# Optimization experiments

Hardware: AMD Instinct MI355X
Metric: run time of the kernel (lower is better)

The kernel has to match this reference:

```python
import jax, jax.numpy as jnp
import numpy as np

_J6 = jnp.array([[0, 0, 0, 0, 0, 1], [0, 0, 0, 0, -1, 0], [0, 0, 0, 1, 0, 0],
                 [0, 0, 1, 0, 0, 0], [0, -1, 0, 0, 0, 0], [1, 0, 0, 0, 0, 0]], dtype=jnp.float32)
_PAIRS4 = [(0, 1), (0, 2), (0, 3), (1, 2), (1, 3), (2, 3)]


def exterior(p1, p2):
    # p1, p2: (B,T,H,4) -> (B,T,H,6) normalized Pluecker line coordinates
    parts = [p1[..., i] * p2[..., j] - p1[..., j] * p2[..., i] for i, j in _PAIRS4]
    L = jnp.stack(parts, axis=-1)
    n = jnp.sqrt(jnp.sum(L * L, axis=-1, keepdims=True))
    return L / jnp.maximum(n, 1e-12)


def setup_inputs() -> dict:
    D, H = 1024, 16
    B, T = 2, 2048
    key = jax.random.key(0)
    ks = jax.random.split(key, 16)
    s = 0.02
    return {
        'x': jax.random.normal(ks[0], (B, T, D), dtype=jnp.float32),
        'qkv_w': jax.random.normal(ks[1], (D, 3 * D), dtype=jnp.float32) * s,
        'qkv_b': jnp.zeros((3 * D,), dtype=jnp.float32),
        'w1_write': jax.random.normal(ks[2], (D, 4 * H), dtype=jnp.float32) * s,
        'w2_write': jax.random.normal(ks[3], (D, 4 * H), dtype=jnp.float32) * s,
        'w1_read': jax.random.normal(ks[4], (D, 4 * H), dtype=jnp.float32) * s,
        'w2_read': jax.random.normal(ks[5], (D, 4 * H), dtype=jnp.float32) * s,
        'geo_w': jax.random.normal(ks[6], (D, D), dtype=jnp.float32) * s,
        'geo_b': jnp.zeros((D,), dtype=jnp.float32),
        'gate_w': jax.random.normal(ks[7], (D, H), dtype=jnp.float32) * s,
        'gate_b': jnp.zeros((H,), dtype=jnp.float32),
        'inc_scale': jnp.ones((H,), dtype=jnp.float32),
        'out_w': jax.random.normal(ks[8], (D, D), dtype=jnp.float32) * s,
        'out_b': jnp.zeros((D,), dtype=jnp.float32),
    }


def reference(x, qkv_w, qkv_b, w1_write, w2_write, w1_read, w2_read,
              geo_w, geo_b, gate_w, gate_b, inc_scale, out_w, out_b):
    B, T, D = x.shape
    H = inc_scale.shape[0]
    dh = D // H
    scale = dh ** -0.5

    qkv = (x @ qkv_w + qkv_b).reshape(B, T, 3, H, dh)
    qkv = jnp.transpose(qkv, (2, 0, 3, 1, 4))  # (3,B,H,T,dh)
    q, k, v = qkv[0], qkv[1], qkv[2]

    std_logits = jnp.einsum('bhqd,bhkd->bhqk', q, k) * scale

    x_prev = jnp.concatenate([jnp.zeros((B, 1, D), dtype=x.dtype), x[:, :-1]], axis=1)
    w1 = (x_prev @ w1_write).reshape(B, T, H, 4)
    w2 = (x @ w2_write).reshape(B, T, H, 4)
    write_lines = exterior(w1, w2)  # (B,T,H,6)
    r1 = (x @ w1_read).reshape(B, T, H, 4)
    r2 = (x @ w2_read).reshape(B, T, H, 4)
    read_lines = exterior(r1, r2)  # (B,T,H,6)

    J_write = jnp.einsum('bthi,ij->bthj', write_lines, _J6)  # (B,T,H,6)
    geo_logits = jnp.einsum('bqhi,bkhi->bhqk', read_lines, J_write)
    geo_logits = geo_logits * inc_scale.reshape(1, H, 1, 1)

    mask = jnp.triu(jnp.ones((T, T), dtype=bool), k=1)  # True above diagonal
    neg = jnp.float32(-jnp.inf)

    std_attn = jax.nn.softmax(jnp.where(mask, neg, std_logits), axis=-1)
    std_out = jnp.einsum('bhqk,bhkd->bqhd', std_attn, v).reshape(B, T, D)

    geo_attn = jax.nn.softmax(jnp.where(mask, neg, geo_logits), axis=-1)
    geo_v = (x @ geo_w + geo_b).reshape(B, T, H, dh)
    geo_out = jnp.einsum('bhqk,bkhd->bqhd', geo_attn, geo_v).reshape(B, T, D)

    gate = jax.nn.sigmoid(x @ gate_w + gate_b)  # (B,T,H)
    gate = jnp.mean(gate, axis=-1, keepdims=True)  # (B,T,1)

    combined = (1.0 - gate) * std_out + gate * geo_out
    return combined @ out_w + out_b
```

## Files before the change

kernel.cpp:

```cpp
#include <hip/hip_runtime.h>
#include <hip/hip_bf16.h>

#define Bc 2
#define Tc 2048
#define Dc 1024
#define Hc 16
#define Mc (Bc*Tc)
#define QB 64
#define KB 32
#define NALL 4480

typedef __attribute__((ext_vector_type(8))) short bf16x8;
typedef __attribute__((ext_vector_type(4))) short bf16x4;
typedef __attribute__((ext_vector_type(4))) float fx4;

__device__ __forceinline__ short f2bf(float f) {
  __hip_bfloat16 h = __float2bfloat16(f);
  return *reinterpret_cast<short*>(&h);
}
__device__ __forceinline__ float bf2f(short s) {
  unsigned int u = ((unsigned int)(unsigned short)s) << 16;
  float f;
  __builtin_memcpy(&f, &u, 4);
  return f;
}

#define MFMA(a, b, c) __builtin_amdgcn_mfma_f32_16x16x32_bf16((a), (b), (c), 0, 0, 0)

#define GLD16(G, L) __builtin_amdgcn_global_load_lds( \
    (const __attribute__((address_space(1))) unsigned int*)(G), \
    (__attribute__((address_space(3))) unsigned int*)(L), 16, 0, 0)

__global__ __launch_bounds__(256) void f2b_k(const float* __restrict__ in,
                                             short* __restrict__ out) {
  const int i = blockIdx.x * 256 + threadIdx.x;
  const float4 v = ((const float4*)in)[i];
  bf16x4 o;
  o[0] = f2bf(v.x); o[1] = f2bf(v.y); o[2] = f2bf(v.z); o[3] = f2bf(v.w);
  ((bf16x4*)out)[i] = o;
}

__global__ void biasall_k(const float* __restrict__ qkv_b,
                          const float* __restrict__ geob,
                          const float* __restrict__ gateb,
                          float* __restrict__ ball) {
  const int n = blockIdx.x * 256 + threadIdx.x;
  if (n >= NALL) return;
  float v = 0.f;
  if (n < 1024)      v = qkv_b[n] * 0.125f;
  else if (n < 3072) v = qkv_b[n];
  else if (n < 4096) v = geob[n - 3072];
  else if (n >= 4352 && n < 4368) v = gateb[n - 4352];
  ball[n] = v;
}

__global__ __launch_bounds__(256) void tconv_all_k(
    const float* __restrict__ qkv_w, const float* __restrict__ geow,
    const float* __restrict__ w1w, const float* __restrict__ w2w,
    const float* __restrict__ w1r, const float* __restrict__ w2r,
    const float* __restrict__ gatew, short* __restrict__ wtall)
{
  __shared__ float tile[32][33];
  const int n0 = blockIdx.x * 32, k0 = blockIdx.y * 32;
  const int tx = threadIdx.x & 31, ty = threadIdx.x >> 5;
  const int n = n0 + tx;
  const float* src = nullptr; int ln = 0, sN = 0;
  if (n < 3072)      { src = qkv_w; ln = n;        sN = 3072; }
  else if (n < 4096) { src = geow;  ln = n - 3072; sN = 1024; }
  else if (n < 4160) { src = w1w;   ln = n - 4096; sN = 64; }
  else if (n < 4224) { src = w2w;   ln = n - 4160; sN = 64; }
  else if (n < 4288) { src = w1r;   ln = n - 4224; sN = 64; }
  else if (n < 4352) { src = w2r;   ln = n - 4288; sN = 64; }
  else if (n < 4368) { src = gatew; ln = n - 4352; sN = 16; }
  #pragma unroll
  for (int i = 0; i < 4; i++)
    tile[ty * 4 + i][tx] = src ? src[(size_t)(k0 + ty * 4 + i) * sN + ln] : 0.f;
  __syncthreads();
  #pragma unroll
  for (int i = 0; i < 4; i++) {
    const int nn = n0 + ty * 4 + i;
    const float s = (nn < 1024) ? 0.125f : 1.f;
    wtall[(size_t)nn * 1024 + k0 + tx] = f2bf(tile[tx][ty * 4 + i] * s);
  }
}

__global__ __launch_bounds__(256) void tconv_k(const float* __restrict__ W,
                                               short* __restrict__ Wt,
                                               int K, int N) {
  __shared__ float tile[32][33];
  const int k0 = blockIdx.y * 32, n0 = blockIdx.x * 32;
  const int tx = threadIdx.x & 31, ty = threadIdx.x >> 5;
  #pragma unroll
  for (int i = 0; i < 4; i++)
    tile[ty * 4 + i][tx] = W[(size_t)(k0 + ty * 4 + i) * N + n0 + tx];
  __syncthreads();
  #pragma unroll
  for (int i = 0; i < 4; i++)
    Wt[(size_t)(n0 + ty * 4 + i) * K + k0 + tx] = f2bf(tile[tx][ty * 4 + i]);
}

template<bool BF16_OUT>
__global__ __launch_bounds__(256) void gemm_mfma_k(
    const short* __restrict__ A, const short* __restrict__ Bt,
    const float* __restrict__ bias, void* __restrict__ Cv,
    int M, int N, int K)
{
  __shared__ short As[128][32];
  __shared__ short Bs[128][32];
  const int m0 = blockIdx.y * 128, n0 = blockIdx.x * 128;
  const int tid = threadIdx.x;
  const int wave = tid >> 6, lane = tid & 63;
  const int l15 = lane & 15, lg = lane >> 4;
  const int wm = wave >> 1, wn = wave & 1;
  const int srow = lane >> 2;
  const int schk = (lane & 3) * 8;

  const size_t aBase = (size_t)(m0 + wave * 16 + srow) * K + schk;
  const size_t bBase = (size_t)(n0 + wave * 16 + srow) * K + schk;

  fx4 acc[4][4] = {};

  for (int k0 = 0; k0 < K; k0 += 32) {
    __syncthreads();
    GLD16(&A[aBase + k0],              &As[wave * 16][0]);
    GLD16(&A[aBase + (size_t)64 * K + k0], &As[64 + wave * 16][0]);
    GLD16(&Bt[bBase + k0],             &Bs[wave * 16][0]);
    GLD16(&Bt[bBase + (size_t)64 * K + k0], &Bs[64 + wave * 16][0]);
    __syncthreads();
    bf16x8 af[4], bf[4];
    #pragma unroll
    for (int i = 0; i < 4; i++) {
      af[i] = *(const bf16x8*)&As[wm * 64 + i * 16 + l15][8 * lg];
      bf[i] = *(const bf16x8*)&Bs[wn * 64 + i * 16 + l15][8 * lg];
    }
    #pragma unroll
    for (int i = 0; i < 4; i++)
      #pragma unroll
      for (int j = 0; j < 4; j++)
        acc[i][j] = MFMA(af[i], bf[j], acc[i][j]);
  }

  #pragma unroll
  for (int i = 0; i < 4; i++)
    #pragma unroll
    for (int j = 0; j < 4; j++) {
      const int n = n0 + wn * 64 + j * 16 + l15;
      const float bv = bias ? bias[n] : 0.f;
      #pragma unroll
      for (int rg = 0; rg < 4; rg++) {
        const int m = m0 + wm * 64 + i * 16 + lg * 4 + rg;
        const float v = acc[i][j][rg] + bv;
        if constexpr (BF16_OUT)
          ((short*)Cv)[(size_t)m * N + n] = f2bf(v);
        else
          ((float*)Cv)[(size_t)m * N + n] = v;
      }
    }
}

__device__ __forceinline__ void exterior6(const float a[4], const float c[4], float L[6]) {
  L[0] = a[0]*c[1] - a[1]*c[0];
  L[1] = a[0]*c[2] - a[2]*c[0];
  L[2] = a[0]*c[3] - a[3]*c[0];
  L[3] = a[1]*c[2] - a[2]*c[1];
  L[4] = a[1]*c[3] - a[3]*c[1];
  L[5] = a[2]*c[3] - a[3]*c[2];
}

__device__ __forceinline__ void load4bf(const short* p, float o[4]) {
  const bf16x4 v = *(const bf16x4*)p;
  o[0] = bf2f(v[0]); o[1] = bf2f(v[1]); o[2] = bf2f(v[2]); o[3] = bf2f(v[3]);
}

__global__ void lines_k(const short* __restrict__ allb,
                        const float* __restrict__ incs,
                        short* __restrict__ JWb, short* __restrict__ RLb)
{
  const int idx = blockIdx.x * 256 + threadIdx.x;
  if (idx >= Bc * Tc * Hc) return;
  const int h = idx & 15;
  const int t = (idx >> 4) & (Tc - 1);
  const int b = idx >> 15;
  const size_t row = (size_t)b * Tc + t;
  const size_t lrow = ((size_t)(b * Hc + h) * Tc + t) * 8;

  float a[4] = {0.f, 0.f, 0.f, 0.f};
  float c[4];
  load4bf(&allb[row * NALL + 4160 + h * 4], c);
  if (t > 0) load4bf(&allb[(row - 1) * NALL + 4096 + h * 4], a);

  float L[6];
  exterior6(a, c, L);
  float n = sqrtf(L[0]*L[0] + L[1]*L[1] + L[2]*L[2] + L[3]*L[3] + L[4]*L[4] + L[5]*L[5]);
  float inv = 1.f / fmaxf(n, 1e-12f);
  const float s = incs[h];
  bf16x8 jw;
  jw[0] = f2bf( L[5] * inv * s);
  jw[1] = f2bf(-L[4] * inv * s);
  jw[2] = f2bf( L[3] * inv * s);
  jw[3] = f2bf( L[2] * inv * s);
  jw[4] = f2bf(-L[1] * inv * s);
  jw[5] = f2bf( L[0] * inv * s);
  jw[6] = 0; jw[7] = 0;
  *(bf16x8*)&JWb[lrow] = jw;

  load4bf(&allb[row * NALL + 4224 + h * 4], a);
  load4bf(&allb[row * NALL + 4288 + h * 4], c);
  exterior6(a, c, L);
  n = sqrtf(L[0]*L[0] + L[1]*L[1] + L[2]*L[2] + L[3]*L[3] + L[4]*L[4] + L[5]*L[5]);
  inv = 1.f / fmaxf(n, 1e-12f);
  bf16x8 rl;
  #pragma unroll
  for (int i = 0; i < 6; i++) rl[i] = f2bf(L[i] * inv);
  rl[6] = 0; rl[7] = 0;
  *(bf16x8*)&RLb[lrow] = rl;
}

__global__ void gate_k(const short* __restrict__ allb, float* __restrict__ gate) {
  const int idx = blockIdx.x * 256 + threadIdx.x;
  if (idx >= Mc) return;
  float ssum = 0.f;
  #pragma unroll
  for (int hh = 0; hh < 16; hh++) {
    const float v = bf2f(allb[(size_t)idx * NALL + 4352 + hh]);
    ssum += 1.f / (1.f + __expf(-v));
  }
  gate[idx] = ssum * (1.f / 16.f);
}

#define LOADK(K0, a0, a1, b0, b1) { \
  const size_t rb0 = (size_t)(b * Tc + (K0) + l15) * NALL + 1024 + h * 64; \
  const size_t rb1 = rb0 + (size_t)16 * NALL; \
  a0 = *(const bf16x8*)&allb[rb0 + lg * 8]; \
  a1 = *(const bf16x8*)&allb[rb0 + 32 + lg * 8]; \
  b0 = *(const bf16x8*)&allb[rb1 + lg * 8]; \
  b1 = *(const bf16x8*)&allb[rb1 + 32 + lg * 8]; }

#define LOADJW(K0, j0, j1) { \
  j0 = z8; j1 = z8; \
  if (lg == 0) { \
    j0 = *(const bf16x8*)&JWb[(size_t)(bh * Tc + (K0) + l15) * 8]; \
    j1 = *(const bf16x8*)&JWb[(size_t)(bh * Tc + (K0) + 16 + l15) * 8]; \
  } }

#define LOADVG(K0, vr, gr) { \
  vr = *(const bf16x8*)&allb[(size_t)(b * Tc + (K0) + kk) * NALL + 2048 + h * 64 + dg]; \
  gr = *(const bf16x8*)&allb[(size_t)(b * Tc + (K0) + kk) * NALL + 3072 + h * 64 + dg]; }

#define STAGEVG(CUR, vr, gr) { \
  _Pragma("unroll") for (int j = 0; j < 8; j++) { \
    const int d = dg + j; \
    const int col = ((kc2 ^ ((d >> 3) & 3)) << 3) | kl2; \
    Vt[CUR][d][col] = vr[j]; Gt[CUR][d][col] = gr[j]; \
  } }

#define COMPUTE(K0, CUR, ka0, ka1, kb0, kb1, jw0, jw1) \
  if ((K0) <= qhi) { \
    fx4 z = {0.f, 0.f, 0.f, 0.f}; \
    fx4 sS0, sS1, sG0, sG1; \
    __builtin_amdgcn_s_setprio(1); \
    sS0 = MFMA(qf0, ka0, z); sS0 = MFMA(qf1, ka1, sS0); \
    sS1 = MFMA(qf0, kb0, z); sS1 = MFMA(qf1, kb1, sS1); \
    sG0 = MFMA(rlf, jw0, z); sG1 = MFMA(rlf, jw1, z); \
    __builtin_amdgcn_s_setprio(0); \
    if ((K0) + KB - 1 > q0 + wave * 16) { \
      const int kg0 = (K0) + l15, kg1 = (K0) + 16 + l15; \
      _Pragma("unroll") for (int r = 0; r < 4; r++) { \
        const int qg = q0 + wave * 16 + lg * 4 + r; \
        if (kg0 > qg) { sS0[r] = -1e30f; sG0[r] = -1e30f; } \
        if (kg1 > qg) { sS1[r] = -1e30f; sG1[r] = -1e30f; } \
      } } \
    _Pragma("unroll") for (int r = 0; r < 4; r++) { \
      const int ql = lg * 4 + r; \
      const float p0 = __expf(sS0[r]); const float p1 = __expf(sS1[r]); \
      lpS[r] += p0 + p1; \
      Ps[wave][ql][l15] = f2bf(p0); Ps[wave][ql][16 + l15] = f2bf(p1); \
      const float g0 = __expf(sG0[r]); const float g1 = __expf(sG1[r]); \
      lpG[r] += g0 + g1; \
      Pg[wave][ql][l15] = f2bf(g0); Pg[wave][ql][16 + l15] = f2bf(g1); \
    } \
    const bf16x8 pa  = *(const bf16x8*)&Ps[wave][l15][8 * lg]; \
    const bf16x8 pga = *(const bf16x8*)&Pg[wave][l15][8 * lg]; \
    __builtin_amdgcn_s_setprio(1); \
    _Pragma("unroll") for (int dt = 0; dt < 4; dt++) { \
      const int dV = dt * 16 + l15; \
      const int swz = 8 * (lg ^ ((dV >> 3) & 3)); \
      accS[dt] = MFMA(pa,  *(const bf16x8*)&Vt[CUR][dV][swz], accS[dt]); \
      accG[dt] = MFMA(pga, *(const bf16x8*)&Gt[CUR][dV][swz], accG[dt]); \
    } \
    __builtin_amdgcn_s_setprio(0); \
  }

__global__ __launch_bounds__(256) void attn3_k(
    const short* __restrict__ allb,
    const short* __restrict__ RLb,
    const short* __restrict__ JWb,
    const float* __restrict__ gate,
    short* __restrict__ combb)
{
  const int orig = blockIdx.x;
  const int xcd  = orig & 7;
  const int idx  = orig >> 3;
  const int pairIdx = idx & 15;
  const int bh   = xcd + 8 * (idx >> 4);
  const int b = bh >> 4, h = bh & 15;
  const int tid = threadIdx.x;
  const int wave = tid >> 6;
  const int lane = tid & 63;
  const int l15 = lane & 15;
  const int lg  = lane >> 4;
  const int kk  = tid >> 3;
  const int dg  = (tid & 7) * 8;
  const int kc2 = kk >> 3, kl2 = kk & 7;

  __shared__ short Vt[2][64][40];
  __shared__ short Gt[2][64][40];
  __shared__ short Ps[4][16][40];
  __shared__ short Pg[4][16][40];

  const bf16x8 z8 = {0, 0, 0, 0, 0, 0, 0, 0};

  for (int half = 0; half < 2; half++) {
    const int qt = half ? (31 - pairIdx) : pairIdx;
    const int q0 = qt * QB;
    const int nkt = 2 * qt + 2;
    const int qrow = wave * 16 + l15;
    const int qhi = q0 + wave * 16 + 15;

    const size_t qrb = (size_t)(b * Tc + q0 + qrow) * NALL + h * 64;
    const bf16x8 qf0 = *(const bf16x8*)&allb[qrb + lg * 8];
    const bf16x8 qf1 = *(const bf16x8*)&allb[qrb + 32 + lg * 8];
    bf16x8 rlf = z8;
    if (lg == 0) rlf = *(const bf16x8*)&RLb[(size_t)(bh * Tc + q0 + qrow) * 8];

    fx4 accS[4] = {}, accG[4] = {};
    float lpS[4] = {0.f, 0.f, 0.f, 0.f};
    float lpG[4] = {0.f, 0.f, 0.f, 0.f};

    bf16x8 kA0a, kA1a, kB0a, kB1a, jw0a, jw1a, vrA, grA;
    bf16x8 kA0b, kA1b, kB0b, kB1b, jw0b, jw1b, vrB, grB;
    LOADK(0, kA0a, kA1a, kB0a, kB1a);
    LOADJW(0, jw0a, jw1a);
    LOADVG(0, vrA, grA);

    __syncthreads();

    for (int kt = 0; kt < nkt; kt += 2) {
      const int k0a = kt * KB, k0b = k0a + KB;
      STAGEVG(0, vrA, grA);
      LOADK(k0b, kA0b, kA1b, kB0b, kB1b);
      LOADJW(k0b, jw0b, jw1b);
      LOADVG(k0b, vrB, grB);
      __syncthreads();
      COMPUTE(k0a, 0, kA0a, kA1a, kB0a, kB1a, jw0a, jw1a);
      STAGEVG(1, vrB, grB);
      if (kt + 2 < nkt) {
        LOADK(k0b + KB, kA0a, kA1a, kB0a, kB1a);
        LOADJW(k0b + KB, jw0a, jw1a);
        LOADVG(k0b + KB, vrA, grA);
      }
      __syncthreads();
      COMPUTE(k0b, 1, kA0b, kA1b, kB0b, kB1b, jw0b, jw1b);
    }

    #pragma unroll
    for (int r = 0; r < 4; r++) {
      float ls = lpS[r];
      ls += __shfl_xor(ls, 1); ls += __shfl_xor(ls, 2);
      ls += __shfl_xor(ls, 4); ls += __shfl_xor(ls, 8);
      float lgeo = lpG[r];
      lgeo += __shfl_xor(lgeo, 1); lgeo += __shfl_xor(lgeo, 2);
      lgeo += __shfl_xor(lgeo, 4); lgeo += __shfl_xor(lgeo, 8);
      const int qg = q0 + wave * 16 + lg * 4 + r;
      const float gt = gate[(size_t)b * Tc + qg];
      const float invS = (1.f - gt) / ls;
      const float invG = gt / lgeo;
      #pragma unroll
      for (int dt = 0; dt < 4; dt++) {
        const float o = accS[dt][r] * invS + accG[dt][r] * invG;
        combb[(size_t)(b * Tc + qg) * 1024 + h * 64 + dt * 16 + l15] = f2bf(o);
      }
    }
  }
}

extern "C" void kernel_launch(void* const* d_in, const int* in_sizes, int n_in,
                              void* d_out, int out_size, void* d_ws, size_t ws_size,
                              hipStream_t stream) {
  (void)in_sizes; (void)n_in; (void)out_size; (void)ws_size;
  const float* x     = (const float*)d_in[0];
  const float* qkv_w = (const float*)d_in[1];
  const float* qkv_b = (const float*)d_in[2];
  const float* w1w   = (const float*)d_in[3];
  const float* w2w   = (const float*)d_in[4];
  const float* w1r   = (const float*)d_in[5];
  const float* w2r   = (const float*)d_in[6];
  const float* geow  = (const float*)d_in[7];
  const float* geob  = (const float*)d_in[8];
  const float* gatew = (const float*)d_in[9];
  const float* gateb = (const float*)d_in[10];
  const float* incs  = (const float*)d_in[11];
  const float* outw  = (const float*)d_in[12];
  const float* outb  = (const float*)d_in[13];
  float* out = (float*)d_out;

  char* p = (char*)d_ws;
  short* xb    = (short*)p;  p += (size_t)4096 * 1024 * 2;
  short* wtall = (short*)p;  p += (size_t)NALL * 1024 * 2;
  short* allb  = (short*)p;  p += (size_t)4096 * NALL * 2;
  short* combb = (short*)p;  p += (size_t)4096 * 1024 * 2;
  short* wtout = (short*)p;  p += (size_t)1024 * 1024 * 2;
  short* JWb   = (short*)p;  p += (size_t)32 * 2048 * 8 * 2;
  short* RLb   = (short*)p;  p += (size_t)32 * 2048 * 8 * 2;
  float* ball  = (float*)p;  p += (size_t)NALL * 4;
  float* gatev = (float*)p;  p += (size_t)4096 * 4;

  const dim3 blk(256);

  f2b_k<<<dim3(4096), blk, 0, stream>>>(x, xb);
  biasall_k<<<dim3((NALL + 255) / 256), blk, 0, stream>>>(qkv_b, geob, gateb, ball);
  tconv_all_k<<<dim3(NALL / 32, 32), blk, 0, stream>>>(qkv_w, geow, w1w, w2w, w1r, w2r, gatew, wtall);
  tconv_k<<<dim3(32, 32), blk, 0, stream>>>(outw, wtout, 1024, 1024);

  gemm_mfma_k<true><<<dim3(NALL / 128, 32), blk, 0, stream>>>(xb, wtall, ball, allb, 4096, NALL, 1024);

  lines_k<<<dim3((Bc * Tc * Hc + 255) / 256), blk, 0, stream>>>(allb, incs, JWb, RLb);
  gate_k<<<dim3((Mc + 255) / 256), blk, 0, stream>>>(allb, gatev);

  attn3_k<<<dim3(512), blk, 0, stream>>>(allb, RLb, JWb, gatev, combb);

  gemm_mfma_k<false><<<dim3(8, 32), blk, 0, stream>>>(combb, wtout, outb, (void*)out, 4096, 1024, 1024);
}
```

Measured before the change: 210.7 us.

## Pre-transpose V/geo-V to global, give each wave its own 32-query tile

Adds a kernel that transposes the V and geo-V slices into a per-head, d-major layout, so the attention kernel can load PV operands directly from global memory into registers instead of staging them through LDS with block-wide barriers. The attention kernel is restructured so each wave independently handles a 32-row query tile (two 16-row subtiles sharing the K loads) with no __syncthreads, and work is balanced by reversing the tile order. Log2e is folded into the Q scale and incidence scale so exp2f replaces __expf. This costs an extra transpose pass and more global reads per wave in exchange for removing synchronization and shared-memory staging.

```diff
diff --git a/kernel.cpp b/kernel.cpp
--- a/kernel.cpp
+++ b/kernel.cpp
@@ -6,9 +6,10 @@
 #define Dc 1024
 #define Hc 16
 #define Mc (Bc*Tc)
-#define QB 64
 #define KB 32
 #define NALL 4480
+#define QSCALE 0.18033688056680776f
+#define LOG2E  1.4426950408889634f
 
 typedef __attribute__((ext_vector_type(8))) short bf16x8;
 typedef __attribute__((ext_vector_type(4))) short bf16x4;
@@ -47,7 +48,7 @@
   const int n = blockIdx.x * 256 + threadIdx.x;
   if (n >= NALL) return;
   float v = 0.f;
-  if (n < 1024)      v = qkv_b[n] * 0.125f;
+  if (n < 1024)      v = qkv_b[n] * QSCALE;
   else if (n < 3072) v = qkv_b[n];
   else if (n < 4096) v = geob[n - 3072];
   else if (n >= 4352 && n < 4368) v = gateb[n - 4352];
@@ -79,7 +80,7 @@
   #pragma unroll
   for (int i = 0; i < 4; i++) {
     const int nn = n0 + ty * 4 + i;
-    const float s = (nn < 1024) ? 0.125f : 1.f;
+    const float s = (nn < 1024) ? QSCALE : 1.f;
     wtall[(size_t)nn * 1024 + k0 + tx] = f2bf(tile[tx][ty * 4 + i] * s);
   }
 }
@@ -158,6 +159,29 @@
     }
 }
 
+__global__ __launch_bounds__(256) void vgt_k(const short* __restrict__ allb,
+                                             short* __restrict__ vgt) {
+  const int t0 = blockIdx.x * 64;
+  const int bh = blockIdx.y;
+  const int path = blockIdx.z;
+  const int b = bh >> 4, h = bh & 15;
+  __shared__ short tile[64][66];
+  const int tt = threadIdx.x >> 2;
+  const int dc = (threadIdx.x & 3) * 16;
+  const size_t src = (size_t)(b * Tc + t0 + tt) * NALL + (path ? 3072 : 2048) + h * 64 + dc;
+  *(bf16x8*)&tile[tt][dc]     = *(const bf16x8*)&allb[src];
+  *(bf16x8*)&tile[tt][dc + 8] = *(const bf16x8*)&allb[src + 8];
+  __syncthreads();
+  const int dd = threadIdx.x >> 2;
+  const int tc = (threadIdx.x & 3) * 16;
+  bf16x8 o0, o1;
+  #pragma unroll
+  for (int j = 0; j < 8; j++) { o0[j] = tile[tc + j][dd]; o1[j] = tile[tc + 8 + j][dd]; }
+  const size_t dst = ((size_t)(path * 32 + bh) * 64 + dd) * Tc + t0 + tc;
+  *(bf16x8*)&vgt[dst]     = o0;
+  *(bf16x8*)&vgt[dst + 8] = o1;
+}
+
 __device__ __forceinline__ void exterior6(const float a[4], const float c[4], float L[6]) {
   L[0] = a[0]*c[1] - a[1]*c[0];
   L[1] = a[0]*c[2] - a[2]*c[0];
@@ -193,7 +217,7 @@
   exterior6(a, c, L);
   float n = sqrtf(L[0]*L[0] + L[1]*L[1] + L[2]*L[2] + L[3]*L[3] + L[4]*L[4] + L[5]*L[5]);
   float inv = 1.f / fmaxf(n, 1e-12f);
-  const float s = incs[h];
+  const float s = incs[h] * LOG2E;
   bf16x8 jw;
   jw[0] = f2bf( L[5] * inv * s);
   jw[1] = f2bf(-L[4] * inv * s);
@@ -228,160 +252,153 @@
   gate[idx] = ssum * (1.f / 16.f);
 }
 
-#define LOADK(K0, a0, a1, b0, b1) { \
+#define LOADKJ4(K0, k00, k01, k10, k11, j0, j1) { \
   const size_t rb0 = (size_t)(b * Tc + (K0) + l15) * NALL + 1024 + h * 64; \
   const size_t rb1 = rb0 + (size_t)16 * NALL; \
-  a0 = *(const bf16x8*)&allb[rb0 + lg * 8]; \
-  a1 = *(const bf16x8*)&allb[rb0 + 32 + lg * 8]; \
-  b0 = *(const bf16x8*)&allb[rb1 + lg * 8]; \
-  b1 = *(const bf16x8*)&allb[rb1 + 32 + lg * 8]; }
-
-#define LOADJW(K0, j0, j1) { \
+  k00 = *(const bf16x8*)&allb[rb0 + lg * 8]; \
+  k01 = *(const bf16x8*)&allb[rb0 + 32 + lg * 8]; \
+  k10 = *(const bf16x8*)&allb[rb1 + lg * 8]; \
+  k11 = *(const bf16x8*)&allb[rb1 + 32 + lg * 8]; \
   j0 = z8; j1 = z8; \
   if (lg == 0) { \
     j0 = *(const bf16x8*)&JWb[(size_t)(bh * Tc + (K0) + l15) * 8]; \
     j1 = *(const bf16x8*)&JWb[(size_t)(bh * Tc + (K0) + 16 + l15) * 8]; \
   } }
 
-#define LOADVG(K0, vr, gr) { \
-  vr = *(const bf16x8*)&allb[(size_t)(b * Tc + (K0) + kk) * NALL + 2048 + h * 64 + dg]; \
-  gr = *(const bf16x8*)&allb[(size_t)(b * Tc + (K0) + kk) * NALL + 3072 + h * 64 + dg]; }
-
-#define STAGEVG(CUR, vr, gr) { \
-  _Pragma("unroll") for (int j = 0; j < 8; j++) { \
-    const int d = dg + j; \
-    const int col = ((kc2 ^ ((d >> 3) & 3)) << 3) | kl2; \
-    Vt[CUR][d][col] = vr[j]; Gt[CUR][d][col] = gr[j]; \
-  } }
-
-#define COMPUTE(K0, CUR, ka0, ka1, kb0, kb1, jw0, jw1) \
-  if ((K0) <= qhi) { \
-    fx4 z = {0.f, 0.f, 0.f, 0.f}; \
-    fx4 sS0, sS1, sG0, sG1; \
-    __builtin_amdgcn_s_setprio(1); \
-    sS0 = MFMA(qf0, ka0, z); sS0 = MFMA(qf1, ka1, sS0); \
-    sS1 = MFMA(qf0, kb0, z); sS1 = MFMA(qf1, kb1, sS1); \
-    sG0 = MFMA(rlf, jw0, z); sG1 = MFMA(rlf, jw1, z); \
-    __builtin_amdgcn_s_setprio(0); \
-    if ((K0) + KB - 1 > q0 + wave * 16) { \
-      const int kg0 = (K0) + l15, kg1 = (K0) + 16 + l15; \
+#define LOADVG4(K0, vf, gf) { \
+  const size_t vb = ((size_t)bh * 64 + l15) * Tc + (K0) + lg * 8; \
+  const size_t gb = vb + (size_t)32 * 64 * Tc; \
+  vf[0] = *(const bf16x8*)&vgt[vb]; \
+  vf[1] = *(const bf16x8*)&vgt[vb + (size_t)16 * Tc]; \
+  vf[2] = *(const bf16x8*)&vgt[vb + (size_t)32 * Tc]; \
+  vf[3] = *(const bf16x8*)&vgt[vb + (size_t)48 * Tc]; \
+  gf[0] = *(const bf16x8*)&vgt[gb]; \
+  gf[1] = *(const bf16x8*)&vgt[gb + (size_t)16 * Tc]; \
+  gf[2] = *(const bf16x8*)&vgt[gb + (size_t)32 * Tc]; \
+  gf[3] = *(const bf16x8*)&vgt[gb + (size_t)48 * Tc]; }
+
+#define COMPUTE4(K0, k00, k01, k10, k11, j0, j1, vf, gf) { \
+  const fx4 z = {0.f, 0.f, 0.f, 0.f}; \
+  fx4 sS[2][2], sG[2][2]; \
+  __builtin_amdgcn_s_setprio(1); \
+  sS[0][0] = MFMA(qf[0][0], k00, z); sS[0][0] = MFMA(qf[0][1], k01, sS[0][0]); \
+  sS[0][1] = MFMA(qf[0][0], k10, z); sS[0][1] = MFMA(qf[0][1], k11, sS[0][1]); \
+  sS[1][0] = MFMA(qf[1][0], k00, z); sS[1][0] = MFMA(qf[1][1], k01, sS[1][0]); \
+  sS[1][1] = MFMA(qf[1][0], k10, z); sS[1][1] = MFMA(qf[1][1], k11, sS[1][1]); \
+  sG[0][0] = MFMA(rlf[0], j0, z); sG[0][1] = MFMA(rlf[0], j1, z); \
+  sG[1][0] = MFMA(rlf[1], j0, z); sG[1][1] = MFMA(rlf[1], j1, z); \
+  __builtin_amdgcn_s_setprio(0); \
+  if ((K0) == q0) { \
+    _Pragma("unroll") for (int sq = 0; sq < 2; sq++) \
+    _Pragma("unroll") for (int st = 0; st < 2; st++) { \
+      const int kg = (K0) + st * 16 + l15; \
       _Pragma("unroll") for (int r = 0; r < 4; r++) { \
-        const int qg = q0 + wave * 16 + lg * 4 + r; \
-        if (kg0 > qg) { sS0[r] = -1e30f; sG0[r] = -1e30f; } \
-        if (kg1 > qg) { sS1[r] = -1e30f; sG1[r] = -1e30f; } \
-      } } \
+        const int qg = q0 + sq * 16 + lg * 4 + r; \
+        if (kg > qg) { sS[sq][st][r] = -1e30f; sG[sq][st][r] = -1e30f; } \
+      } } } \
+  _Pragma("unroll") for (int sq = 0; sq < 2; sq++) { \
     _Pragma("unroll") for (int r = 0; r < 4; r++) { \
       const int ql = lg * 4 + r; \
-      const float p0 = __expf(sS0[r]); const float p1 = __expf(sS1[r]); \
-      lpS[r] += p0 + p1; \
-      Ps[wave][ql][l15] = f2bf(p0); Ps[wave][ql][16 + l15] = f2bf(p1); \
-      const float g0 = __expf(sG0[r]); const float g1 = __expf(sG1[r]); \
-      lpG[r] += g0 + g1; \
-      Pg[wave][ql][l15] = f2bf(g0); Pg[wave][ql][16 + l15] = f2bf(g1); \
-    } \
-    const bf16x8 pa  = *(const bf16x8*)&Ps[wave][l15][8 * lg]; \
-    const bf16x8 pga = *(const bf16x8*)&Pg[wave][l15][8 * lg]; \
-    __builtin_amdgcn_s_setprio(1); \
+      const float p0 = exp2f(sS[sq][0][r]); \
+      const float p1 = exp2f(sS[sq][1][r]); \
+      lpS[sq][r] += p0 + p1; \
+      Ps[wave][sq][ql][l15]      = f2bf(p0); \
+      Ps[wave][sq][ql][16 + l15] = f2bf(p1); \
+      const float g0 = exp2f(sG[sq][0][r]); \
+      const float g1 = exp2f(sG[sq][1][r]); \
+      lpG[sq][r] += g0 + g1; \
+      Pg[wave][sq][ql][l15]      = f2bf(g0); \
+      Pg[wave][sq][ql][16 + l15] = f2bf(g1); \
+    } } \
+  __builtin_amdgcn_s_setprio(1); \
+  _Pragma("unroll") for (int sq = 0; sq < 2; sq++) { \
+    const bf16x8 pa  = *(const bf16x8*)&Ps[wave][sq][l15][8 * lg]; \
+    const bf16x8 pga = *(const bf16x8*)&Pg[wave][sq][l15][8 * lg]; \
     _Pragma("unroll") for (int dt = 0; dt < 4; dt++) { \
-      const int dV = dt * 16 + l15; \
-      const int swz = 8 * (lg ^ ((dV >> 3) & 3)); \
-      accS[dt] = MFMA(pa,  *(const bf16x8*)&Vt[CUR][dV][swz], accS[dt]); \
-      accG[dt] = MFMA(pga, *(const bf16x8*)&Gt[CUR][dV][swz], accG[dt]); \
-    } \
-    __builtin_amdgcn_s_setprio(0); \
-  }
-
-__global__ __launch_bounds__(256) void attn3_k(
+      accS[sq][dt] = MFMA(pa,  vf[dt], accS[sq][dt]); \
+      accG[sq][dt] = MFMA(pga, gf[dt], accG[sq][dt]); \
+    } } \
+  __builtin_amdgcn_s_setprio(0); }
+
+__global__ __launch_bounds__(256) void attn4_k(
     const short* __restrict__ allb,
+    const short* __restrict__ vgt,
     const short* __restrict__ RLb,
     const short* __restrict__ JWb,
     const float* __restrict__ gate,
     short* __restrict__ combb)
 {
   const int orig = blockIdx.x;
-  const int xcd  = orig & 7;
-  const int idx  = orig >> 3;
-  const int pairIdx = idx & 15;
-  const int bh   = xcd + 8 * (idx >> 4);
+  const int xcd = orig & 7;
+  const int g = orig >> 3;
+  const int bh = xcd + 8 * (g >> 4);
+  const int blkIn = g & 15;
+  const int tid = threadIdx.x;
+  const int wave = tid >> 6, lane = tid & 63;
+  const int l15 = lane & 15, lg = lane >> 4;
+  const int qs = 63 - (blkIn * 4 + wave);
   const int b = bh >> 4, h = bh & 15;
-  const int tid = threadIdx.x;
-  const int wave = tid >> 6;
-  const int lane = tid & 63;
-  const int l15 = lane & 15;
-  const int lg  = lane >> 4;
-  const int kk  = tid >> 3;
-  const int dg  = (tid & 7) * 8;
-  const int kc2 = kk >> 3, kl2 = kk & 7;
-
-  __shared__ short Vt[2][64][40];
-  __shared__ short Gt[2][64][40];
-  __shared__ short Ps[4][16][40];
-  __shared__ short Pg[4][16][40];
+  const int q0 = qs * 32;
+
+  __shared__ short Ps[4][2][16][40];
+  __shared__ short Pg[4][2][16][40];
 
   const bf16x8 z8 = {0, 0, 0, 0, 0, 0, 0, 0};
 
-  for (int half = 0; half < 2; half++) {
-    const int qt = half ? (31 - pairIdx) : pairIdx;
-    const int q0 = qt * QB;
-    const int nkt = 2 * qt + 2;
-    const int qrow = wave * 16 + l15;
-    const int qhi = q0 + wave * 16 + 15;
-
-    const size_t qrb = (size_t)(b * Tc + q0 + qrow) * NALL + h * 64;
-    const bf16x8 qf0 = *(const bf16x8*)&allb[qrb + lg * 8];
-    const bf16x8 qf1 = *(const bf16x8*)&allb[qrb + 32 + lg * 8];
-    bf16x8 rlf = z8;
-    if (lg == 0) rlf = *(const bf16x8*)&RLb[(size_t)(bh * Tc + q0 + qrow) * 8];
-
-    fx4 accS[4] = {}, accG[4] = {};
-    float lpS[4] = {0.f, 0.f, 0.f, 0.f};
-    float lpG[4] = {0.f, 0.f, 0.f, 0.f};
-
-    bf16x8 kA0a, kA1a, kB0a, kB1a, jw0a, jw1a, vrA, grA;
-    bf16x8 kA0b, kA1b, kB0b, kB1b, jw0b, jw1b, vrB, grB;
-    LOADK(0, kA0a, kA1a, kB0a, kB1a);
-    LOADJW(0, jw0a, jw1a);
-    LOADVG(0, vrA, grA);
-
-    __syncthreads();
-
-    for (int kt = 0; kt < nkt; kt += 2) {
-      const int k0a = kt * KB, k0b = k0a + KB;
-      STAGEVG(0, vrA, grA);
-      LOADK(k0b, kA0b, kA1b, kB0b, kB1b);
-      LOADJW(k0b, jw0b, jw1b);
-      LOADVG(k0b, vrB, grB);
-      __syncthreads();
-      COMPUTE(k0a, 0, kA0a, kA1a, kB0a, kB1a, jw0a, jw1a);
-      STAGEVG(1, vrB, grB);
-      if (kt + 2 < nkt) {
-        LOADK(k0b + KB, kA0a, kA1a, kB0a, kB1a);
-        LOADJW(k0b + KB, jw0a, jw1a);
-        LOADVG(k0b + KB, vrA, grA);
-      }
-      __syncthreads();
-      COMPUTE(k0b, 1, kA0b, kA1b, kB0b, kB1b, jw0b, jw1b);
+  bf16x8 qf[2][2], rlf[2];
+  #pragma unroll
+  for (int sq = 0; sq < 2; sq++) {
+    const size_t qrb = (size_t)(b * Tc + q0 + sq * 16 + l15) * NALL + h * 64;
+    qf[sq][0] = *(const bf16x8*)&allb[qrb + lg * 8];
+    qf[sq][1] = *(const bf16x8*)&allb[qrb + 32 + lg * 8];
+    rlf[sq] = z8;
+    if (lg == 0)
+      rlf[sq] = *(const bf16x8*)&RLb[(size_t)(bh * Tc + q0 + sq * 16 + l15) * 8];
+  }
+
+  fx4 accS[2][4] = {}, accG[2][4] = {};
+  float lpS[2][4] = {}, lpG[2][4] = {};
+
+  bf16x8 kA00, kA01, kA10, kA11, jA0, jA1;
+  bf16x8 kB00, kB01, kB10, kB11, jB0, jB1;
+  LOADKJ4(0, kA00, kA01, kA10, kA11, jA0, jA1);
+
+  const int nkt = qs + 1;
+  for (int kt = 0; kt < nkt; kt += 2) {
+    {
+      bf16x8 vf[4], gf[4];
+      LOADVG4(kt * KB, vf, gf);
+      if (kt + 1 < nkt) LOADKJ4((kt + 1) * KB, kB00, kB01, kB10, kB11, jB0, jB1);
+      COMPUTE4(kt * KB, kA00, kA01, kA10, kA11, jA0, jA1, vf, gf);
     }
-
+    if (kt + 1 < nkt) {
+      bf16x8 vf[4], gf[4];
+      LOADVG4((kt + 1) * KB, vf, gf);
+      if (kt + 2 < nkt) LOADKJ4((kt + 2) * KB, kA00, kA01, kA10, kA11, jA0, jA1);
+      COMPUTE4((kt + 1) * KB, kB00, kB01, kB10, kB11, jB0, jB1, vf, gf);
+    }
+  }
+
+  #pragma unroll
+  for (int sq = 0; sq < 2; sq++)
     #pragma unroll
     for (int r = 0; r < 4; r++) {
-      float ls = lpS[r];
+      float ls = lpS[sq][r];
       ls += __shfl_xor(ls, 1); ls += __shfl_xor(ls, 2);
       ls += __shfl_xor(ls, 4); ls += __shfl_xor(ls, 8);
-      float lgeo = lpG[r];
+      float lgeo = lpG[sq][r];
       lgeo += __shfl_xor(lgeo, 1); lgeo += __shfl_xor(lgeo, 2);
       lgeo += __shfl_xor(lgeo, 4); lgeo += __shfl_xor(lgeo, 8);
-      const int qg = q0 + wave * 16 + lg * 4 + r;
+      const int qg = q0 + sq * 16 + lg * 4 + r;
       const float gt = gate[(size_t)b * Tc + qg];
       const float invS = (1.f - gt) / ls;
       const float invG = gt / lgeo;
       #pragma unroll
       for (int dt = 0; dt < 4; dt++) {
-        const float o = accS[dt][r] * invS + accG[dt][r] * invG;
+        const float o = accS[sq][dt][r] * invS + accG[sq][dt][r] * invG;
         combb[(size_t)(b * Tc + qg) * 1024 + h * 64 + dt * 16 + l15] = f2bf(o);
       }
     }
-  }
 }
 
 extern "C" void kernel_launch(void* const* d_in, const int* in_sizes, int n_in,
@@ -408,6 +425,7 @@
   short* xb    = (short*)p;  p += (size_t)4096 * 1024 * 2;
   short* wtall = (short*)p;  p += (size_t)NALL * 1024 * 2;
   short* allb  = (short*)p;  p += (size_t)4096 * NALL * 2;
+  short* vgt   = (short*)p;  p += (size_t)2 * 32 * 64 * Tc * 2;
   short* combb = (short*)p;  p += (size_t)4096 * 1024 * 2;
   short* wtout = (short*)p;  p += (size_t)1024 * 1024 * 2;
   short* JWb   = (short*)p;  p += (size_t)32 * 2048 * 8 * 2;
@@ -424,10 +442,11 @@
 
   gemm_mfma_k<true><<<dim3(NALL / 128, 32), blk, 0, stream>>>(xb, wtall, ball, allb, 4096, NALL, 1024);
 
+  vgt_k<<<dim3(Tc / 64, 32, 2), blk, 0, stream>>>(allb, vgt);
   lines_k<<<dim3((Bc * Tc * Hc + 255) / 256), blk, 0, stream>>>(allb, incs, JWb, RLb);
   gate_k<<<dim3((Mc + 255) / 256), blk, 0, stream>>>(allb, gatev);
 
-  attn3_k<<<dim3(512), blk, 0, stream>>>(allb, RLb, JWb, gatev, combb);
+  attn4_k<<<dim3(512), blk, 0, stream>>>(allb, vgt, RLb, JWb, gatev, combb);
 
   gemm_mfma_k<false><<<dim3(8, 32), blk, 0, stream>>>(combb, wtout, outb, (void*)out, 4096, 1024, 1024);
 }
```

After: 291.2 us. +38.2%, slower.

## Pre-transpose V and geo-V, stage via direct global-to-LDS loads, use exp2

Applied to the files above, without the earlier changes.

Adds a kernel that writes V and geo_v into a d-major (transposed) buffer. The attention kernel can then fill its LDS tiles with direct global-to-LDS loads using a rotated swizzle, instead of register loads followed by scattered LDS stores. The pipeline is reordered so the next tile's loads are issued before the current compute, with one barrier per step. The query scale and the inc_scale are folded with log2(e) so the kernel can call exp2f instead of __expf. The cost is an extra launch and an extra pass over V/G memory.

```diff
diff --git a/kernel.cpp b/kernel.cpp
--- a/kernel.cpp
+++ b/kernel.cpp
@@ -6,9 +6,10 @@
 #define Dc 1024
 #define Hc 16
 #define Mc (Bc*Tc)
-#define QB 64
 #define KB 32
 #define NALL 4480
+#define QSCALE 0.18033688056680776f
+#define LOG2E  1.4426950408889634f
 
 typedef __attribute__((ext_vector_type(8))) short bf16x8;
 typedef __attribute__((ext_vector_type(4))) short bf16x4;
@@ -47,7 +48,7 @@
   const int n = blockIdx.x * 256 + threadIdx.x;
   if (n >= NALL) return;
   float v = 0.f;
-  if (n < 1024)      v = qkv_b[n] * 0.125f;
+  if (n < 1024)      v = qkv_b[n] * QSCALE;
   else if (n < 3072) v = qkv_b[n];
   else if (n < 4096) v = geob[n - 3072];
   else if (n >= 4352 && n < 4368) v = gateb[n - 4352];
@@ -79,7 +80,7 @@
   #pragma unroll
   for (int i = 0; i < 4; i++) {
     const int nn = n0 + ty * 4 + i;
-    const float s = (nn < 1024) ? 0.125f : 1.f;
+    const float s = (nn < 1024) ? QSCALE : 1.f;
     wtall[(size_t)nn * 1024 + k0 + tx] = f2bf(tile[tx][ty * 4 + i] * s);
   }
 }
@@ -158,6 +159,29 @@
     }
 }
 
+__global__ __launch_bounds__(256) void vgt_k(const short* __restrict__ allb,
+                                             short* __restrict__ vgt) {
+  const int t0 = blockIdx.x * 64;
+  const int bh = blockIdx.y;
+  const int path = blockIdx.z;
+  const int b = bh >> 4, h = bh & 15;
+  __shared__ short tile[64][66];
+  const int tt = threadIdx.x >> 2;
+  const int dc = (threadIdx.x & 3) * 16;
+  const size_t src = (size_t)(b * Tc + t0 + tt) * NALL + (path ? 3072 : 2048) + h * 64 + dc;
+  *(bf16x8*)&tile[tt][dc]     = *(const bf16x8*)&allb[src];
+  *(bf16x8*)&tile[tt][dc + 8] = *(const bf16x8*)&allb[src + 8];
+  __syncthreads();
+  const int dd = threadIdx.x >> 2;
+  const int tc = (threadIdx.x & 3) * 16;
+  bf16x8 o0, o1;
+  #pragma unroll
+  for (int j = 0; j < 8; j++) { o0[j] = tile[tc + j][dd]; o1[j] = tile[tc + 8 + j][dd]; }
+  const size_t dst = ((size_t)(path * 32 + bh) * 64 + dd) * Tc + t0 + tc;
+  *(bf16x8*)&vgt[dst]     = o0;
+  *(bf16x8*)&vgt[dst + 8] = o1;
+}
+
 __device__ __forceinline__ void exterior6(const float a[4], const float c[4], float L[6]) {
   L[0] = a[0]*c[1] - a[1]*c[0];
   L[1] = a[0]*c[2] - a[2]*c[0];
@@ -193,7 +217,7 @@
   exterior6(a, c, L);
   float n = sqrtf(L[0]*L[0] + L[1]*L[1] + L[2]*L[2] + L[3]*L[3] + L[4]*L[4] + L[5]*L[5]);
   float inv = 1.f / fmaxf(n, 1e-12f);
-  const float s = incs[h];
+  const float s = incs[h] * LOG2E;
   bf16x8 jw;
   jw[0] = f2bf( L[5] * inv * s);
   jw[1] = f2bf(-L[4] * inv * s);
@@ -228,40 +252,31 @@
   gate[idx] = ssum * (1.f / 16.f);
 }
 
-#define LOADK(K0, a0, a1, b0, b1) { \
+#define LOADKJ(K0, k00, k01, k10, k11, j0, j1) { \
   const size_t rb0 = (size_t)(b * Tc + (K0) + l15) * NALL + 1024 + h * 64; \
   const size_t rb1 = rb0 + (size_t)16 * NALL; \
-  a0 = *(const bf16x8*)&allb[rb0 + lg * 8]; \
-  a1 = *(const bf16x8*)&allb[rb0 + 32 + lg * 8]; \
-  b0 = *(const bf16x8*)&allb[rb1 + lg * 8]; \
-  b1 = *(const bf16x8*)&allb[rb1 + 32 + lg * 8]; }
-
-#define LOADJW(K0, j0, j1) { \
+  k00 = *(const bf16x8*)&allb[rb0 + lg * 8]; \
+  k01 = *(const bf16x8*)&allb[rb0 + 32 + lg * 8]; \
+  k10 = *(const bf16x8*)&allb[rb1 + lg * 8]; \
+  k11 = *(const bf16x8*)&allb[rb1 + 32 + lg * 8]; \
   j0 = z8; j1 = z8; \
   if (lg == 0) { \
     j0 = *(const bf16x8*)&JWb[(size_t)(bh * Tc + (K0) + l15) * 8]; \
     j1 = *(const bf16x8*)&JWb[(size_t)(bh * Tc + (K0) + 16 + l15) * 8]; \
   } }
 
-#define LOADVG(K0, vr, gr) { \
-  vr = *(const bf16x8*)&allb[(size_t)(b * Tc + (K0) + kk) * NALL + 2048 + h * 64 + dg]; \
-  gr = *(const bf16x8*)&allb[(size_t)(b * Tc + (K0) + kk) * NALL + 3072 + h * 64 + dg]; }
-
-#define STAGEVG(CUR, vr, gr) { \
-  _Pragma("unroll") for (int j = 0; j < 8; j++) { \
-    const int d = dg + j; \
-    const int col = ((kc2 ^ ((d >> 3) & 3)) << 3) | kl2; \
-    Vt[CUR][d][col] = vr[j]; Gt[CUR][d][col] = gr[j]; \
-  } }
-
-#define COMPUTE(K0, CUR, ka0, ka1, kb0, kb1, jw0, jw1) \
+#define GSTAGE(CUR, K0) { \
+  GLD16(&vgt[vgbase + (K0)], &Vt[CUR][wave * 16][0]); \
+  GLD16(&vgt[vgbase + GOFF + (K0)], &Gt[CUR][wave * 16][0]); }
+
+#define COMPUTE(K0, CUR, k00, k01, k10, k11, j0, j1) \
   if ((K0) <= qhi) { \
-    fx4 z = {0.f, 0.f, 0.f, 0.f}; \
+    const fx4 z = {0.f, 0.f, 0.f, 0.f}; \
     fx4 sS0, sS1, sG0, sG1; \
     __builtin_amdgcn_s_setprio(1); \
-    sS0 = MFMA(qf0, ka0, z); sS0 = MFMA(qf1, ka1, sS0); \
-    sS1 = MFMA(qf0, kb0, z); sS1 = MFMA(qf1, kb1, sS1); \
-    sG0 = MFMA(rlf, jw0, z); sG1 = MFMA(rlf, jw1, z); \
+    sS0 = MFMA(qf0, k00, z); sS0 = MFMA(qf1, k01, sS0); \
+    sS1 = MFMA(qf0, k10, z); sS1 = MFMA(qf1, k11, sS1); \
+    sG0 = MFMA(rlf, j0, z);  sG1 = MFMA(rlf, j1, z); \
     __builtin_amdgcn_s_setprio(0); \
     if ((K0) + KB - 1 > q0 + wave * 16) { \
       const int kg0 = (K0) + l15, kg1 = (K0) + 16 + l15; \
@@ -272,10 +287,10 @@
       } } \
     _Pragma("unroll") for (int r = 0; r < 4; r++) { \
       const int ql = lg * 4 + r; \
-      const float p0 = __expf(sS0[r]); const float p1 = __expf(sS1[r]); \
+      const float p0 = exp2f(sS0[r]); const float p1 = exp2f(sS1[r]); \
       lpS[r] += p0 + p1; \
       Ps[wave][ql][l15] = f2bf(p0); Ps[wave][ql][16 + l15] = f2bf(p1); \
-      const float g0 = __expf(sG0[r]); const float g1 = __expf(sG1[r]); \
+      const float g0 = exp2f(sG0[r]); const float g1 = exp2f(sG1[r]); \
       lpG[r] += g0 + g1; \
       Pg[wave][ql][l15] = f2bf(g0); Pg[wave][ql][16 + l15] = f2bf(g1); \
     } \
@@ -284,15 +299,15 @@
     __builtin_amdgcn_s_setprio(1); \
     _Pragma("unroll") for (int dt = 0; dt < 4; dt++) { \
       const int dV = dt * 16 + l15; \
-      const int swz = 8 * (lg ^ ((dV >> 3) & 3)); \
-      accS[dt] = MFMA(pa,  *(const bf16x8*)&Vt[CUR][dV][swz], accS[dt]); \
-      accG[dt] = MFMA(pga, *(const bf16x8*)&Gt[CUR][dV][swz], accG[dt]); \
+      accS[dt] = MFMA(pa,  *(const bf16x8*)&Vt[CUR][dV][rpos], accS[dt]); \
+      accG[dt] = MFMA(pga, *(const bf16x8*)&Gt[CUR][dV][rpos], accG[dt]); \
     } \
     __builtin_amdgcn_s_setprio(0); \
   }
 
-__global__ __launch_bounds__(256) void attn3_k(
+__global__ __launch_bounds__(256) void attn5_k(
     const short* __restrict__ allb,
+    const short* __restrict__ vgt,
     const short* __restrict__ RLb,
     const short* __restrict__ JWb,
     const float* __restrict__ gate,
@@ -309,20 +324,23 @@
   const int lane = tid & 63;
   const int l15 = lane & 15;
   const int lg  = lane >> 4;
-  const int kk  = tid >> 3;
-  const int dg  = (tid & 7) * 8;
-  const int kc2 = kk >> 3, kl2 = kk & 7;
-
-  __shared__ short Vt[2][64][40];
-  __shared__ short Gt[2][64][40];
+
+  __shared__ short Vt[2][64][32];
+  __shared__ short Gt[2][64][32];
   __shared__ short Ps[4][16][40];
   __shared__ short Pg[4][16][40];
 
   const bf16x8 z8 = {0, 0, 0, 0, 0, 0, 0, 0};
 
+  const int srow = wave * 16 + (lane >> 2);
+  const int schunk = ((lane & 3) - (srow >> 1)) & 3;
+  const size_t vgbase = ((size_t)bh * 64 + srow) * Tc + schunk * 8;
+  const size_t GOFF = (size_t)32 * 64 * Tc;
+  const int rpos = ((lg + (l15 >> 1)) & 3) * 8;
+
   for (int half = 0; half < 2; half++) {
     const int qt = half ? (31 - pairIdx) : pairIdx;
-    const int q0 = qt * QB;
+    const int q0 = qt * 64;
     const int nkt = 2 * qt + 2;
     const int qrow = wave * 16 + l15;
     const int qhi = q0 + wave * 16 + 15;
@@ -337,30 +355,24 @@
     float lpS[4] = {0.f, 0.f, 0.f, 0.f};
     float lpG[4] = {0.f, 0.f, 0.f, 0.f};
 
-    bf16x8 kA0a, kA1a, kB0a, kB1a, jw0a, jw1a, vrA, grA;
-    bf16x8 kA0b, kA1b, kB0b, kB1b, jw0b, jw1b, vrB, grB;
-    LOADK(0, kA0a, kA1a, kB0a, kB1a);
-    LOADJW(0, jw0a, jw1a);
-    LOADVG(0, vrA, grA);
-
+    bf16x8 kA00, kA01, kA10, kA11, jA0, jA1;
+    bf16x8 kB00, kB01, kB10, kB11, jB0, jB1;
+
+    GSTAGE(0, 0);
+    LOADKJ(0, kA00, kA01, kA10, kA11, jA0, jA1);
     __syncthreads();
 
     for (int kt = 0; kt < nkt; kt += 2) {
-      const int k0a = kt * KB, k0b = k0a + KB;
-      STAGEVG(0, vrA, grA);
-      LOADK(k0b, kA0b, kA1b, kB0b, kB1b);
-      LOADJW(k0b, jw0b, jw1b);
-      LOADVG(k0b, vrB, grB);
+      GSTAGE(1, (kt + 1) * KB);
+      LOADKJ((kt + 1) * KB, kB00, kB01, kB10, kB11, jB0, jB1);
+      COMPUTE(kt * KB, 0, kA00, kA01, kA10, kA11, jA0, jA1);
       __syncthreads();
-      COMPUTE(k0a, 0, kA0a, kA1a, kB0a, kB1a, jw0a, jw1a);
-      STAGEVG(1, vrB, grB);
       if (kt + 2 < nkt) {
-        LOADK(k0b + KB, kA0a, kA1a, kB0a, kB1a);
-        LOADJW(k0b + KB, jw0a, jw1a);
-        LOADVG(k0b + KB, vrA, grA);
+        GSTAGE(0, (kt + 2) * KB);
+        LOADKJ((kt + 2) * KB, kA00, kA01, kA10, kA11, jA0, jA1);
       }
+      COMPUTE((kt + 1) * KB, 1, kB00, kB01, kB10, kB11, jB0, jB1);
       __syncthreads();
-      COMPUTE(k0b, 1, kA0b, kA1b, kB0b, kB1b, jw0b, jw1b);
     }
 
     #pragma unroll
@@ -408,6 +420,7 @@
   short* xb    = (short*)p;  p += (size_t)4096 * 1024 * 2;
   short* wtall = (short*)p;  p += (size_t)NALL * 1024 * 2;
   short* allb  = (short*)p;  p += (size_t)4096 * NALL * 2;
+  short* vgt   = (short*)p;  p += (size_t)2 * 32 * 64 * Tc * 2;
   short* combb = (short*)p;  p += (size_t)4096 * 1024 * 2;
   short* wtout = (short*)p;  p += (size_t)1024 * 1024 * 2;
   short* JWb   = (short*)p;  p += (size_t)32 * 2048 * 8 * 2;
@@ -424,10 +437,11 @@
 
   gemm_mfma_k<true><<<dim3(NALL / 128, 32), blk, 0, stream>>>(xb, wtall, ball, allb, 4096, NALL, 1024);
 
+  vgt_k<<<dim3(Tc / 64, 32, 2), blk, 0, stream>>>(allb, vgt);
   lines_k<<<dim3((Bc * Tc * Hc + 255) / 256), blk, 0, stream>>>(allb, incs, JWb, RLb);
   gate_k<<<dim3((Mc + 255) / 256), blk, 0, stream>>>(allb, gatev);
 
-  attn3_k<<<dim3(512), blk, 0, stream>>>(allb, RLb, JWb, gatev, combb);
+  attn5_k<<<dim3(512), blk, 0, stream>>>(allb, vgt, RLb, JWb, gatev, combb);
 
   gemm_mfma_k<false><<<dim3(8, 32), blk, 0, stream>>>(combb, wtout, outb, (void*)out, 4096, 1024, 1024);
 }
```

After: 217.4 us. 3.2% more time.
